# Kernel tuning notes

Hardware: AMD Instinct MI355X
Metric: run time of the kernel (lower is better)

The kernel has to match this reference:

```python
import jax, jax.numpy as jnp
import numpy as np

NEG_INF = -1e9

def _build_tables():
    # LC0-style 73-plane encoding per from-square: planes 0..55 queen moves
    # (8 directions x 7 distances), 56..63 knight moves. to_sq[from, plane]
    # is the to-square index; valid marks on-board targets.
    to_sq = np.zeros((64, 64), np.int32)
    valid = np.zeros((64, 64), bool)
    dirs = [(1, 0), (1, 1), (0, 1), (-1, 1), (-1, 0), (-1, -1), (0, -1), (1, -1)]
    knights = [(2, 1), (1, 2), (-1, 2), (-2, 1), (-2, -1), (-1, -2), (1, -2), (2, -1)]
    for sq in range(64):
        r, c = divmod(sq, 8)
        for d, (dr, dc) in enumerate(dirs):
            for dist in range(1, 8):
                p = d * 7 + (dist - 1)
                nr, nc = r + dr * dist, c + dc * dist
                if 0 <= nr < 8 and 0 <= nc < 8:
                    to_sq[sq, p] = nr * 8 + nc
                    valid[sq, p] = True
        for i, (dr, dc) in enumerate(knights):
            nr, nc = r + dr, c + dc
            if 0 <= nr < 8 and 0 <= nc < 8:
                to_sq[sq, 56 + i] = nr * 8 + nc
                valid[sq, 56 + i] = True
    promo_from = (np.arange(64) // 8) == 6  # rank 7 pawns (0-indexed rank 6)
    return to_sq, valid, promo_from

TO_SQ_NP, VALID_NP, PROMO_FROM_NP = _build_tables()
TO_SQ = jnp.asarray(TO_SQ_NP)            # (64, 64) int32
TO_VALID = jnp.asarray(VALID_NP)         # (64, 64) bool
PROMO_FROM = jnp.asarray(PROMO_FROM_NP)  # (64,) bool

EMBED_DIM = 1024
POLICY_DIM = 128
SCALE = POLICY_DIM ** (-0.5)


def setup_inputs() -> dict:
    key = jax.random.key(0)
    ks = jax.random.split(key, 4)
    B = 1024
    std = 1.0 / np.sqrt(EMBED_DIM)
    x = jax.random.normal(ks[0], (B, 64, EMBED_DIM), dtype=jnp.float32)
    Wq = jax.random.normal(ks[1], (EMBED_DIM, POLICY_DIM), dtype=jnp.float32) * std
    Wk = jax.random.normal(ks[2], (EMBED_DIM, POLICY_DIM), dtype=jnp.float32) * std
    Wu = jax.random.normal(ks[3], (EMBED_DIM, 9), dtype=jnp.float32) * std
    bq = jnp.zeros((POLICY_DIM,), jnp.float32)
    bk = jnp.zeros((POLICY_DIM,), jnp.float32)
    bu = jnp.zeros((9,), jnp.float32)
    return {"x": x, "Wq": Wq, "bq": bq, "Wk": Wk, "bk": bk, "Wu": Wu, "bu": bu}


def reference(x, Wq, bq, Wk, bk, Wu, bu):
    b = x.shape[0]
    q = jnp.einsum('bsd,dp->bsp', x, Wq) + bq            # (B, 64, P)
    k = jnp.einsum('bsd,dp->bsp', x, Wk) + bk            # (B, 64, P)
    logits_ft = jnp.einsum('bfp,btp->bft', q, k) * SCALE  # (B, 64, 64)
    # gather to-square logits into plane order per from-square
    idx = jnp.broadcast_to(TO_SQ[None].astype(jnp.int32), (b, 64, 64))
    logits_64 = jnp.take_along_axis(logits_ft, idx, axis=-1)  # (B, 64, 64)
    logits_64 = jnp.where(TO_VALID[None], logits_64, jnp.float32(NEG_INF))
    up = jnp.einsum('bsd,dn->bsn', x, Wu) + bu            # (B, 64, 9)
    up = jnp.where(PROMO_FROM[None, :, None], up, jnp.float32(NEG_INF))
    logits = jnp.concatenate([logits_64, up], axis=-1)    # (B, 64, 73)
    return logits.reshape(b, 64 * 73)
```

## Files before the change

kernel.cpp:

```cpp
#include <hip/hip_runtime.h>

#define NEG_INF (-1e9f)
#define SCALE_F 0.08838834764831845f

typedef __attribute__((ext_vector_type(8))) short short8;
typedef __attribute__((ext_vector_type(4))) float float4v;

__device__ __constant__ int cDR[8] = {1,1,0,-1,-1,-1,0,1};
__device__ __constant__ int cDC[8] = {0,1,1,1,0,-1,-1,-1};
__device__ __constant__ int cKR[8] = {2,1,-1,-2,-2,-1,1,2};
__device__ __constant__ int cKC[8] = {1,2,2,1,-1,-2,-2,-1};

__device__ __forceinline__ ushort f2bf(float f) {
  union { float f; unsigned u; } a; a.f = f;
  unsigned u = a.u;
  return (ushort)((u + 0x7FFFu + ((u >> 16) & 1u)) >> 16);
}

__device__ __forceinline__ void glds16(const void* g, void* l) {
  __builtin_amdgcn_global_load_lds(
      (const __attribute__((address_space(1))) unsigned int*)g,
      (__attribute__((address_space(3))) unsigned int*)l, 16, 0, 0);
}

__device__ __forceinline__ short8 pack8(float4 a, float4 b) {
  union { short8 v; unsigned u[4]; } o;
  unsigned a0 = __float_as_uint(a.x), a1 = __float_as_uint(a.y);
  unsigned a2 = __float_as_uint(a.z), a3 = __float_as_uint(a.w);
  unsigned b0 = __float_as_uint(b.x), b1 = __float_as_uint(b.y);
  unsigned b2 = __float_as_uint(b.z), b3 = __float_as_uint(b.w);
  o.u[0] = (a1 & 0xFFFF0000u) | (a0 >> 16);
  o.u[1] = (a3 & 0xFFFF0000u) | (a2 >> 16);
  o.u[2] = (b1 & 0xFFFF0000u) | (b0 >> 16);
  o.u[3] = (b3 & 0xFFFF0000u) | (b2 >> 16);
  return o.v;
}

__global__ void wconv_kernel(const float* __restrict__ Wq,
                             const float* __restrict__ Wk,
                             const float* __restrict__ Wu,
                             ushort* __restrict__ Wsw) {
  int row = blockIdx.x;
  for (int k = threadIdx.x; k < 1024; k += 256) {
    float v;
    if (row < 128)      v = Wq[k * 128 + row];
    else if (row < 256) v = Wk[k * 128 + (row - 128)];
    else if (row < 265) v = Wu[k * 9 + (row - 256)];
    else                v = 0.f;
    int kc = k >> 6, kin = k & 63, seg = kin >> 3, j = kin & 7;
    int sseg = seg ^ (row & 7);
    Wsw[(size_t)kc * 18432 + row * 64 + sseg * 8 + j] = f2bf(v);
  }
}

__global__ __launch_bounds__(256, 3)
void apol_main(const float* __restrict__ x,
               const float* __restrict__ bq,
               const float* __restrict__ bk,
               const float* __restrict__ bu,
               const ushort* __restrict__ Wsw,
               float* __restrict__ out) {
  __shared__ __align__(16) char smem[53248];
  char*   xsB = smem;
  char*   wtB = smem + 16384;
  ushort* qs  = (ushort*)smem;
  ushort* ks  = (ushort*)(smem + 16896);
  float*  Sl  = (float*)smem;

  const int tid = threadIdx.x;
  const int w = tid >> 6, lane = tid & 63;
  const int l15 = lane & 15, qd = lane >> 4;
  const char* xb = (const char*)(x + (size_t)blockIdx.x * 65536);
  const char* WsB = (const char*)Wsw;

  int xsrc[4], xlds[4];
  #pragma unroll
  for (int c = 0; c < 4; ++c) {
    int g = (c * 4 + w) * 64 + lane;
    int row = g >> 4, sg = g & 15;
    xsrc[c] = row * 4096 + ((sg ^ (row & 7)) * 16);
    xlds[c] = (c * 4 + w) * 1024;
  }

  int aaddr[4][2][2];
  #pragma unroll
  for (int mt = 0; mt < 4; ++mt) {
    int row = mt * 16 + l15;
    #pragma unroll
    for (int kk = 0; kk < 2; ++kk)
      #pragma unroll
      for (int h = 0; h < 2; ++h)
        aaddr[mt][kk][h] = row * 256 + (((kk * 8 + qd * 2 + h) ^ (row & 7)) * 16);
  }
  int baddr[4][2], uaddr[2];
  #pragma unroll
  for (int nt = 0; nt < 4; ++nt) {
    int row = w * 64 + nt * 16 + l15;
    #pragma unroll
    for (int kk = 0; kk < 2; ++kk)
      baddr[nt][kk] = row * 128 + (((kk * 4 + qd) ^ (l15 & 7)) * 16);
  }
  #pragma unroll
  for (int kk = 0; kk < 2; ++kk)
    uaddr[kk] = (256 + l15) * 128 + (((kk * 4 + qd) ^ (l15 & 7)) * 16);

  float4v acc[4][4];
  #pragma unroll
  for (int i = 0; i < 4; ++i)
    #pragma unroll
    for (int j = 0; j < 4; ++j)
      acc[i][j] = (float4v){0.f, 0.f, 0.f, 0.f};
  float4v aup = (float4v){0.f, 0.f, 0.f, 0.f};

  #pragma unroll 1
  for (int kc = 0; kc < 16; ++kc) {
    #pragma unroll
    for (int c = 0; c < 4; ++c)
      glds16(xb + kc * 256 + xsrc[c], xsB + xlds[c]);
    const char* wsrc = WsB + (size_t)kc * 36864 + (size_t)lane * 16;
    #pragma unroll
    for (int c = 0; c < 9; ++c)
      glds16(wsrc + (c * 4 + w) * 1024, wtB + (c * 4 + w) * 1024);
    __syncthreads();

    #pragma unroll
    for (int kk = 0; kk < 2; ++kk) {
      short8 af[4];
      #pragma unroll
      for (int mt = 0; mt < 4; ++mt) {
        float4 g0 = *(const float4*)(xsB + aaddr[mt][kk][0]);
        float4 g1 = *(const float4*)(xsB + aaddr[mt][kk][1]);
        af[mt] = pack8(g0, g1);
      }
      short8 bf[4];
      #pragma unroll
      for (int nt = 0; nt < 4; ++nt)
        bf[nt] = *(const short8*)(wtB + baddr[nt][kk]);
      #pragma unroll
      for (int mt = 0; mt < 4; ++mt)
        #pragma unroll
        for (int nt = 0; nt < 4; ++nt)
          acc[mt][nt] = __builtin_amdgcn_mfma_f32_16x16x32_bf16(
              af[mt], bf[nt], acc[mt][nt], 0, 0, 0);
      if (w == 3) {
        short8 ub = *(const short8*)(wtB + uaddr[kk]);
        aup = __builtin_amdgcn_mfma_f32_16x16x32_bf16(af[3], ub, aup, 0, 0, 0);
      }
    }
    __syncthreads();
  }

  float* outb = out + (size_t)blockIdx.x * 4672;

  if (w == 3 && qd < 2 && l15 < 9) {
    float bias = bu[l15];
    #pragma unroll
    for (int r = 0; r < 4; ++r) {
      int f = 48 + qd * 4 + r;
      outb[f * 73 + 64 + l15] = aup[r] + bias;
    }
  }

  #pragma unroll
  for (int nt = 0; nt < 4; ++nt) {
    int C = w * 64 + nt * 16 + l15;
    bool isq = (C < 128);
    int p = isq ? C : (C - 128);
    float bias = isq ? bq[p] : bk[p];
    ushort* dstb = isq ? qs : ks;
    #pragma unroll
    for (int mt = 0; mt < 4; ++mt)
      #pragma unroll
      for (int r = 0; r < 4; ++r) {
        int row = mt * 16 + qd * 4 + r;
        float v = acc[mt][nt][r] + bias;
        if (isq) v *= SCALE_F;
        dstb[row * 132 + p] = f2bf(v);
      }
  }
  __syncthreads();

  float4v acc2[4];
  #pragma unroll
  for (int nt = 0; nt < 4; ++nt) acc2[nt] = (float4v){0.f, 0.f, 0.f, 0.f};
  #pragma unroll
  for (int kp = 0; kp < 4; ++kp) {
    int kb = kp * 32 + qd * 8;
    short8 a2 = *(const short8*)((const char*)&qs[(w * 16 + l15) * 132 + kb]);
    #pragma unroll
    for (int nt = 0; nt < 4; ++nt) {
      short8 b2 = *(const short8*)((const char*)&ks[(nt * 16 + l15) * 132 + kb]);
      acc2[nt] = __builtin_amdgcn_mfma_f32_16x16x32_bf16(a2, b2, acc2[nt], 0, 0, 0);
    }
  }
  __syncthreads();
  #pragma unroll
  for (int nt = 0; nt < 4; ++nt)
    #pragma unroll
    for (int r = 0; r < 4; ++r)
      Sl[(w * 16 + qd * 4 + r) * 65 + nt * 16 + l15] = acc2[nt][r];
  __syncthreads();

  for (int idx = tid; idx < 4672; idx += 256) {
    int f = idx / 73;
    int j = idx - f * 73;
    float val;
    if (j < 64) {
      int rr = f >> 3, cc = f & 7;
      int nr, nc;
      if (j < 56) {
        int d = j / 7;
        int dist = j - d * 7 + 1;
        nr = rr + cDR[d] * dist;
        nc = cc + cDC[d] * dist;
      } else {
        nr = rr + cKR[j - 56];
        nc = cc + cKC[j - 56];
      }
      val = (nr >= 0 && nr < 8 && nc >= 0 && nc < 8) ? Sl[f * 65 + nr * 8 + nc]
                                                     : NEG_INF;
    } else {
      if (f >= 48 && f < 56) continue;
      val = NEG_INF;
    }
    outb[idx] = val;
  }
}

extern "C" void kernel_launch(void* const* d_in, const int* in_sizes, int n_in,
                              void* d_out, int out_size, void* d_ws, size_t ws_size,
                              hipStream_t stream) {
  const float* x  = (const float*)d_in[0];
  const float* Wq = (const float*)d_in[1];
  const float* bq = (const float*)d_in[2];
  const float* Wk = (const float*)d_in[3];
  const float* bk = (const float*)d_in[4];
  const float* Wu = (const float*)d_in[5];
  const float* bu = (const float*)d_in[6];
  float* out = (float*)d_out;
  ushort* Wsw = (ushort*)d_ws;

  const int B = in_sizes[0] / 65536;

  wconv_kernel<<<288, 256, 0, stream>>>(Wq, Wk, Wu, Wsw);
  apol_main<<<B, 256, 0, stream>>>(x, bq, bk, bu, Wsw, out);
}
```

Baseline: 403.0 us.

## Split into 128-row projection GEMM and separate attention/gather kernel

The fused per-batch kernel is split in two. The first kernel computes the Q/K/U projection for two batch items per block (128 rows by 256 columns, K-chunk of 32), so each staged weight tile is reused across twice as many rows. The second kernel computes QK^T and the move gather. Q and K now pass between the kernels through a swizzled bf16 workspace buffer in global memory, which adds an extra launch, a global round trip, and lower occupancy (launch bounds 2) with more accumulators per thread.

```diff
diff --git a/kernel.cpp b/kernel.cpp
--- a/kernel.cpp
+++ b/kernel.cpp
@@ -25,14 +25,10 @@
 
 __device__ __forceinline__ short8 pack8(float4 a, float4 b) {
   union { short8 v; unsigned u[4]; } o;
-  unsigned a0 = __float_as_uint(a.x), a1 = __float_as_uint(a.y);
-  unsigned a2 = __float_as_uint(a.z), a3 = __float_as_uint(a.w);
-  unsigned b0 = __float_as_uint(b.x), b1 = __float_as_uint(b.y);
-  unsigned b2 = __float_as_uint(b.z), b3 = __float_as_uint(b.w);
-  o.u[0] = (a1 & 0xFFFF0000u) | (a0 >> 16);
-  o.u[1] = (a3 & 0xFFFF0000u) | (a2 >> 16);
-  o.u[2] = (b1 & 0xFFFF0000u) | (b0 >> 16);
-  o.u[3] = (b3 & 0xFFFF0000u) | (b2 >> 16);
+  o.u[0] = (__float_as_uint(a.y) & 0xFFFF0000u) | (__float_as_uint(a.x) >> 16);
+  o.u[1] = (__float_as_uint(a.w) & 0xFFFF0000u) | (__float_as_uint(a.z) >> 16);
+  o.u[2] = (__float_as_uint(b.y) & 0xFFFF0000u) | (__float_as_uint(b.x) >> 16);
+  o.u[3] = (__float_as_uint(b.w) & 0xFFFF0000u) | (__float_as_uint(b.z) >> 16);
   return o.v;
 }
 
@@ -47,137 +43,138 @@
     else if (row < 256) v = Wk[k * 128 + (row - 128)];
     else if (row < 265) v = Wu[k * 9 + (row - 256)];
     else                v = 0.f;
-    int kc = k >> 6, kin = k & 63, seg = kin >> 3, j = kin & 7;
-    int sseg = seg ^ (row & 7);
-    Wsw[(size_t)kc * 18432 + row * 64 + sseg * 8 + j] = f2bf(v);
-  }
-}
-
-__global__ __launch_bounds__(256, 3)
-void apol_main(const float* __restrict__ x,
-               const float* __restrict__ bq,
-               const float* __restrict__ bk,
-               const float* __restrict__ bu,
-               const ushort* __restrict__ Wsw,
-               float* __restrict__ out) {
-  __shared__ __align__(16) char smem[53248];
-  char*   xsB = smem;
-  char*   wtB = smem + 16384;
-  ushort* qs  = (ushort*)smem;
-  ushort* ks  = (ushort*)(smem + 16896);
-  float*  Sl  = (float*)smem;
+    int kc = k >> 5, kin = k & 31, g = kin >> 3, j = kin & 7;
+    int sg = g ^ (row & 3);
+    Wsw[(size_t)kc * 9216 + row * 32 + sg * 8 + j] = f2bf(v);
+  }
+}
+
+__global__ __launch_bounds__(256, 2)
+void qk_gemm(const float* __restrict__ x,
+             const float* __restrict__ bq,
+             const float* __restrict__ bk,
+             const float* __restrict__ bu,
+             const ushort* __restrict__ Wsw,
+             ushort* __restrict__ qkbuf,
+             float* __restrict__ out) {
+  __shared__ __align__(16) char smem[34816];
+  char* xsB = smem;
+  char* wtB = smem + 16384;
 
   const int tid = threadIdx.x;
   const int w = tid >> 6, lane = tid & 63;
   const int l15 = lane & 15, qd = lane >> 4;
-  const char* xb = (const char*)(x + (size_t)blockIdx.x * 65536);
-  const char* WsB = (const char*)Wsw;
-
-  int xsrc[4], xlds[4];
+  const int wm = w >> 1, wn = w & 1;
+
+  const char* xb = (const char*)x + (size_t)blockIdx.x * 524288;
+  const char* WsB = (const char*)Wsw + (size_t)lane * 16;
+
+  int xsrc[4];
   #pragma unroll
   for (int c = 0; c < 4; ++c) {
-    int g = (c * 4 + w) * 64 + lane;
-    int row = g >> 4, sg = g & 15;
+    int s = c * 4 + w;
+    int row = s * 8 + (lane >> 3);
+    int sg = lane & 7;
     xsrc[c] = row * 4096 + ((sg ^ (row & 7)) * 16);
-    xlds[c] = (c * 4 + w) * 1024;
-  }
-
-  int aaddr[4][2][2];
-  #pragma unroll
-  for (int mt = 0; mt < 4; ++mt) {
-    int row = mt * 16 + l15;
-    #pragma unroll
-    for (int kk = 0; kk < 2; ++kk)
-      #pragma unroll
-      for (int h = 0; h < 2; ++h)
-        aaddr[mt][kk][h] = row * 256 + (((kk * 8 + qd * 2 + h) ^ (row & 7)) * 16);
-  }
-  int baddr[4][2], uaddr[2];
-  #pragma unroll
-  for (int nt = 0; nt < 4; ++nt) {
-    int row = w * 64 + nt * 16 + l15;
-    #pragma unroll
-    for (int kk = 0; kk < 2; ++kk)
-      baddr[nt][kk] = row * 128 + (((kk * 4 + qd) ^ (l15 & 7)) * 16);
-  }
-  #pragma unroll
-  for (int kk = 0; kk < 2; ++kk)
-    uaddr[kk] = (256 + l15) * 128 + (((kk * 4 + qd) ^ (l15 & 7)) * 16);
-
-  float4v acc[4][4];
+  }
+
+  float4v acc[4][8];
   #pragma unroll
   for (int i = 0; i < 4; ++i)
     #pragma unroll
-    for (int j = 0; j < 4; ++j)
+    for (int j = 0; j < 8; ++j)
       acc[i][j] = (float4v){0.f, 0.f, 0.f, 0.f};
   float4v aup = (float4v){0.f, 0.f, 0.f, 0.f};
 
   #pragma unroll 1
-  for (int kc = 0; kc < 16; ++kc) {
+  for (int kc = 0; kc < 32; ++kc) {
     #pragma unroll
     for (int c = 0; c < 4; ++c)
-      glds16(xb + kc * 256 + xsrc[c], xsB + xlds[c]);
-    const char* wsrc = WsB + (size_t)kc * 36864 + (size_t)lane * 16;
-    #pragma unroll
-    for (int c = 0; c < 9; ++c)
-      glds16(wsrc + (c * 4 + w) * 1024, wtB + (c * 4 + w) * 1024);
+      glds16(xb + kc * 128 + xsrc[c], xsB + (c * 4 + w) * 1024);
+    const char* wsrc = WsB + (size_t)kc * 18432;
+    #pragma unroll
+    for (int c = 0; c < 5; ++c) {
+      int s = c * 4 + w;
+      if (s < 18) glds16(wsrc + s * 1024, wtB + s * 1024);
+    }
     __syncthreads();
 
-    #pragma unroll
-    for (int kk = 0; kk < 2; ++kk) {
-      short8 af[4];
+    short8 af[4];
+    #pragma unroll
+    for (int mt = 0; mt < 4; ++mt) {
+      int row = wm * 64 + mt * 16 + l15;
+      int g0 = qd * 2;
+      float4 v0 = *(const float4*)(xsB + row * 128 + ((g0 ^ (row & 7)) * 16));
+      float4 v1 = *(const float4*)(xsB + row * 128 + (((g0 + 1) ^ (row & 7)) * 16));
+      af[mt] = pack8(v0, v1);
+    }
+    const int gb = (qd ^ (l15 & 3)) * 16;
+    short8 bf[8];
+    #pragma unroll
+    for (int nt = 0; nt < 8; ++nt) {
+      int rowB = wn * 128 + nt * 16 + l15;
+      bf[nt] = *(const short8*)(wtB + rowB * 64 + gb);
+    }
+    #pragma unroll
+    for (int mt = 0; mt < 4; ++mt)
       #pragma unroll
-      for (int mt = 0; mt < 4; ++mt) {
-        float4 g0 = *(const float4*)(xsB + aaddr[mt][kk][0]);
-        float4 g1 = *(const float4*)(xsB + aaddr[mt][kk][1]);
-        af[mt] = pack8(g0, g1);
-      }
-      short8 bf[4];
-      #pragma unroll
-      for (int nt = 0; nt < 4; ++nt)
-        bf[nt] = *(const short8*)(wtB + baddr[nt][kk]);
+      for (int nt = 0; nt < 8; ++nt)
+        acc[mt][nt] = __builtin_amdgcn_mfma_f32_16x16x32_bf16(
+            af[mt], bf[nt], acc[mt][nt], 0, 0, 0);
+    if (wn) {
+      short8 ub = *(const short8*)(wtB + (256 + l15) * 64 + gb);
+      aup = __builtin_amdgcn_mfma_f32_16x16x32_bf16(af[3], ub, aup, 0, 0, 0);
+    }
+    __syncthreads();
+  }
+
+  const int batch = blockIdx.x * 2 + wm;
+
+  if (wn && qd < 2 && l15 < 9) {
+    float bias = bu[l15];
+    #pragma unroll
+    for (int r = 0; r < 4; ++r) {
+      int f = 48 + qd * 4 + r;
+      out[(size_t)batch * 4672 + f * 73 + 64 + l15] = aup[r] + bias;
+    }
+  }
+
+  {
+    const float* bias_ptr = wn ? bk : bq;
+    ushort* dst = qkbuf + (size_t)batch * 16384 + wn * 8192;
+    #pragma unroll
+    for (int nt = 0; nt < 8; ++nt) {
+      int p = nt * 16 + l15;
+      float bias = bias_ptr[p];
+      int g = p >> 3, j = p & 7;
       #pragma unroll
       for (int mt = 0; mt < 4; ++mt)
         #pragma unroll
-        for (int nt = 0; nt < 4; ++nt)
-          acc[mt][nt] = __builtin_amdgcn_mfma_f32_16x16x32_bf16(
-              af[mt], bf[nt], acc[mt][nt], 0, 0, 0);
-      if (w == 3) {
-        short8 ub = *(const short8*)(wtB + uaddr[kk]);
-        aup = __builtin_amdgcn_mfma_f32_16x16x32_bf16(af[3], ub, aup, 0, 0, 0);
-      }
-    }
-    __syncthreads();
-  }
-
-  float* outb = out + (size_t)blockIdx.x * 4672;
-
-  if (w == 3 && qd < 2 && l15 < 9) {
-    float bias = bu[l15];
-    #pragma unroll
-    for (int r = 0; r < 4; ++r) {
-      int f = 48 + qd * 4 + r;
-      outb[f * 73 + 64 + l15] = aup[r] + bias;
-    }
-  }
-
-  #pragma unroll
-  for (int nt = 0; nt < 4; ++nt) {
-    int C = w * 64 + nt * 16 + l15;
-    bool isq = (C < 128);
-    int p = isq ? C : (C - 128);
-    float bias = isq ? bq[p] : bk[p];
-    ushort* dstb = isq ? qs : ks;
-    #pragma unroll
-    for (int mt = 0; mt < 4; ++mt)
-      #pragma unroll
-      for (int r = 0; r < 4; ++r) {
-        int row = mt * 16 + qd * 4 + r;
-        float v = acc[mt][nt][r] + bias;
-        if (isq) v *= SCALE_F;
-        dstb[row * 132 + p] = f2bf(v);
-      }
-  }
+        for (int r = 0; r < 4; ++r) {
+          int f = mt * 16 + qd * 4 + r;
+          float v = acc[mt][nt][r] + bias;
+          if (!wn) v *= SCALE_F;
+          dst[f * 128 + ((g ^ (f & 7)) * 8) + j] = f2bf(v);
+        }
+    }
+  }
+}
+
+__global__ __launch_bounds__(256)
+void attn_gather(const ushort* __restrict__ qkbuf,
+                 float* __restrict__ out) {
+  __shared__ __align__(16) char smem[32768];
+  float* Sl = (float*)smem;
+
+  const int tid = threadIdx.x;
+  const int w = tid >> 6, lane = tid & 63;
+  const int l15 = lane & 15, qd = lane >> 4;
+
+  const char* src = (const char*)qkbuf + (size_t)blockIdx.x * 32768 +
+                    (size_t)lane * 16;
+  #pragma unroll
+  for (int c = 0; c < 8; ++c)
+    glds16(src + (c * 4 + w) * 1024, smem + (c * 4 + w) * 1024);
   __syncthreads();
 
   float4v acc2[4];
@@ -185,11 +182,13 @@
   for (int nt = 0; nt < 4; ++nt) acc2[nt] = (float4v){0.f, 0.f, 0.f, 0.f};
   #pragma unroll
   for (int kp = 0; kp < 4; ++kp) {
-    int kb = kp * 32 + qd * 8;
-    short8 a2 = *(const short8*)((const char*)&qs[(w * 16 + l15) * 132 + kb]);
+    int m = w * 16 + l15;
+    short8 a2 = *(const short8*)(smem + m * 256 + (((kp * 4 + qd) ^ (m & 7)) * 16));
     #pragma unroll
     for (int nt = 0; nt < 4; ++nt) {
-      short8 b2 = *(const short8*)((const char*)&ks[(nt * 16 + l15) * 132 + kb]);
+      int t = nt * 16 + l15;
+      short8 b2 = *(const short8*)(smem + 16384 + t * 256 +
+                                   (((kp * 4 + qd) ^ (t & 7)) * 16));
       acc2[nt] = __builtin_amdgcn_mfma_f32_16x16x32_bf16(a2, b2, acc2[nt], 0, 0, 0);
     }
   }
@@ -201,6 +200,7 @@
       Sl[(w * 16 + qd * 4 + r) * 65 + nt * 16 + l15] = acc2[nt][r];
   __syncthreads();
 
+  float* outb = out + (size_t)blockIdx.x * 4672;
   for (int idx = tid; idx < 4672; idx += 256) {
     int f = idx / 73;
     int j = idx - f * 73;
@@ -238,10 +238,12 @@
   const float* Wu = (const float*)d_in[5];
   const float* bu = (const float*)d_in[6];
   float* out = (float*)d_out;
-  ushort* Wsw = (ushort*)d_ws;
+  ushort* Wsw   = (ushort*)d_ws;
+  ushort* qkbuf = (ushort*)((char*)d_ws + (1 << 20));
 
   const int B = in_sizes[0] / 65536;
 
   wconv_kernel<<<288, 256, 0, stream>>>(Wq, Wk, Wu, Wsw);
-  apol_main<<<B, 256, 0, stream>>>(x, bq, bk, bu, Wsw, out);
-}
+  qk_gemm<<<B / 2, 256, 0, stream>>>(x, bq, bk, bu, Wsw, qkbuf, out);
+  attn_gather<<<B, 256, 0, stream>>>(qkbuf, out);
+}
```

Result: slower. 427.8 us (+6.2%).
